# Optimization experiments

Hardware: AMD Instinct MI355X
Metric: run time of the kernel (lower is better)

Reference implementation:

```python
import jax, jax.numpy as jnp
import numpy as np

NUM_GROUPS = 32
EPS = 1e-6


def setup_inputs() -> dict:
    key = jax.random.key(0)
    ks = jax.random.split(key, 4)
    B, C, H, W = 16, 512, 32, 32
    x = jax.random.normal(ks[0], (B, C, H, W), dtype=jnp.float32)
    norm_w = jnp.ones((C,), dtype=jnp.float32)
    norm_b = jnp.zeros((C,), dtype=jnp.float32)
    qkv_w = jax.random.normal(ks[1], (3 * C, C), dtype=jnp.float32) * (1.0 / np.sqrt(C))
    qkv_b = jnp.zeros((3 * C,), dtype=jnp.float32)
    proj_w = jax.random.normal(ks[2], (C, C), dtype=jnp.float32) * (1.0 / np.sqrt(C))
    proj_b = jnp.zeros((C,), dtype=jnp.float32)
    return {"x": x, "norm_w": norm_w, "norm_b": norm_b, "qkv_w": qkv_w,
            "qkv_b": qkv_b, "proj_w": proj_w, "proj_b": proj_b}


def _group_norm(x, w, b):
    B, C, H, W = x.shape
    g = NUM_GROUPS
    xg = x.reshape(B, g, C // g, H * W)
    mu = xg.mean(axis=(2, 3), keepdims=True)
    var = xg.var(axis=(2, 3), keepdims=True)
    xn = (xg - mu) * jax.lax.rsqrt(var + EPS)
    xn = xn.reshape(B, C, H, W)
    return xn * w[None, :, None, None] + b[None, :, None, None]


def reference(x, norm_w, norm_b, qkv_w, qkv_b, proj_w, proj_b):
    B, C, H, W = x.shape
    h = _group_norm(x, norm_w, norm_b)
    # 1x1 conv == channel GEMM
    qkv = jnp.einsum('oc,bchw->bohw', qkv_w, h) + qkv_b[None, :, None, None]
    q, k, v = jnp.split(qkv, 3, axis=1)
    N = H * W
    q = q.reshape(B, C, N)  # (b, c, n)
    k = k.reshape(B, C, N)
    v = v.reshape(B, C, N)
    scale = jnp.asarray(C, x.dtype) ** -0.5
    attn = jnp.einsum('bci,bcj->bij', q, k) * scale  # (b, Nq, Nk)
    attn = jax.nn.softmax(attn, axis=2)
    o = jnp.einsum('bcj,bij->bci', v, attn).reshape(B, C, H, W)
    out = jnp.einsum('oc,bchw->bohw', proj_w, o) + proj_b[None, :, None, None]
    return x + out
```

## Files before the change

### kernel.cpp

```cpp
#include <hip/hip_runtime.h>

typedef unsigned short u16;
typedef __bf16 bf16x8 __attribute__((ext_vector_type(8)));
typedef float f32x4 __attribute__((ext_vector_type(4)));

#define AS1 __attribute__((address_space(1)))
#define AS3 __attribute__((address_space(3)))


__device__ __forceinline__ u16 f2bf(float f) {
  union { float f; unsigned u; } v; v.f = f;
  return (u16)((v.u + 0x7fffu + ((v.u >> 16) & 1u)) >> 16);
}

__device__ __forceinline__ f32x4 mfma16(bf16x8 a, bf16x8 b, f32x4 c) {
  return __builtin_amdgcn_mfma_f32_16x16x32_bf16(a, b, c, 0, 0, 0);
}

__device__ __forceinline__ void stage_tile(const u16* __restrict__ src, size_t ld,
                                           u16* lds, int wv, int lane) {
#pragma unroll
  for (int h2 = 0; h2 < 2; h2++) {
    int rbase = wv * 32 + h2 * 16;
    int row = rbase + (lane >> 2);
    int segd = (lane & 3) ^ ((row >> 1) & 3);
    __builtin_amdgcn_global_load_lds(
        (const AS1 void*)(src + (size_t)row * ld + segd * 8),
        (AS3 void*)(lds + rbase * 32), 16, 0, 0);
  }
}

__device__ __forceinline__ bf16x8 ldsfrag(const u16* lds, int row, int rowq) {
  int q = rowq ^ ((row >> 1) & 3);
  return *(const bf16x8*)(lds + row * 32 + q * 8);
}

template<int NT>
__device__ __forceinline__ void gemm_core3(const u16* __restrict__ A, int lda,
                                           const u16* __restrict__ B, int ldb,
                                           u16* lds, f32x4 (&acc)[4][4],
                                           int wave, int lane) {
  u16* a0 = lds;         u16* a1 = lds + 4096;  u16* a2 = lds + 8192;
  u16* b0 = lds + 12288; u16* b1 = lds + 16384; u16* b2 = lds + 20480;
  int wm = wave >> 1, wn = wave & 1;
  int col = lane & 15, rq = lane >> 4;
#pragma unroll
  for (int m = 0; m < 4; m++)
#pragma unroll
    for (int n = 0; n < 4; n++) acc[m][n] = (f32x4){0.f, 0.f, 0.f, 0.f};

  stage_tile(A, lda, a0, wave, lane);
  stage_tile(B, ldb, b0, wave, lane);
  stage_tile(A + 32, lda, a1, wave, lane);
  stage_tile(B + 32, ldb, b1, wave, lane);

  for (int t = 0; t < NT; t++) {
    if (t < NT - 1) {
      asm volatile("s_waitcnt vmcnt(4)" ::: "memory");
    } else {
      asm volatile("s_waitcnt vmcnt(0)" ::: "memory");
    }
    __builtin_amdgcn_sched_barrier(0);
    __builtin_amdgcn_s_barrier();
    __builtin_amdgcn_sched_barrier(0);
    if (t + 2 < NT) {
      stage_tile(A + (size_t)(t + 2) * 32, lda, a2, wave, lane);
      stage_tile(B + (size_t)(t + 2) * 32, ldb, b2, wave, lane);
    }
    bf16x8 af[4], bfr[4];
#pragma unroll
    for (int n = 0; n < 4; n++) bfr[n] = ldsfrag(b0, wn * 64 + n * 16 + col, rq);
#pragma unroll
    for (int m = 0; m < 4; m++) af[m] = ldsfrag(a0, wm * 64 + m * 16 + col, rq);
#pragma unroll
    for (int m = 0; m < 4; m++)
#pragma unroll
      for (int n = 0; n < 4; n++) acc[m][n] = mfma16(af[m], bfr[n], acc[m][n]);
    u16* ta = a0; a0 = a1; a1 = a2; a2 = ta;
    u16* tb = b0; b0 = b1; b1 = b2; b2 = tb;
  }
}

__device__ __forceinline__ void epi_flush(const u16* lds, u16* gdst, size_t stride, int t) {
#pragma unroll
  for (int pass = 0; pass < 8; pass++) {
    int row = pass * 16 + (t >> 4);
    int ch = (t & 15) * 8;
    uint4 w = *(const uint4*)(lds + row * 132 + ch);
    *(uint4*)(gdst + (size_t)row * stride + ch) = w;
  }
}

__device__ __forceinline__ void stage_half(const u16* __restrict__ src, size_t ld,
                                           u16* ldsbase, int wave, int lane) {
#pragma unroll
  for (int r = 0; r < 2; r++) {
    int rb = (r * 8 + wave) * 8;
    int row = rb + (lane >> 3);
    int seg = (lane & 7) ^ (row & 7);
    __builtin_amdgcn_global_load_lds(
        (const AS1 void*)(src + (size_t)row * ld + seg * 8),
        (AS3 void*)(ldsbase + rb * 64), 16, 0, 0);
  }
}

template<int P>
__device__ __forceinline__ void phase_read(const u16* cA, const u16* cB,
                                           bf16x8 (&af)[2][2], bf16x8 (&bfr)[4][2],
                                           int wm, int wn, int col, int rq) {
  if constexpr (P == 0) {
#pragma unroll
    for (int nf = 0; nf < 4; nf++)
#pragma unroll
      for (int kk = 0; kk < 2; kk++) {
        int row = wn * 64 + nf * 16 + col;
        bfr[nf][kk] = *(const bf16x8*)(cB + row * 64 + (((kk << 2) + rq) ^ (row & 7)) * 8);
      }
  }
#pragma unroll
  for (int i = 0; i < 2; i++)
#pragma unroll
    for (int kk = 0; kk < 2; kk++) {
      int row = wm * 128 + (P * 2 + i) * 16 + col;
      af[i][kk] = *(const bf16x8*)(cA + row * 64 + (((kk << 2) + rq) ^ (row & 7)) * 8);
    }
}

template<int P>
__device__ __forceinline__ void phase_fma(const bf16x8 (&af)[2][2],
                                          const bf16x8 (&bfr)[4][2],
                                          f32x4 (&acc)[8][4]) {
#pragma unroll
  for (int i = 0; i < 2; i++)
#pragma unroll
    for (int kk = 0; kk < 2; kk++)
#pragma unroll
      for (int nf = 0; nf < 4; nf++)
        acc[P * 2 + i][nf] = mfma16(af[i][kk], bfr[nf][kk], acc[P * 2 + i][nf]);
}

#define RUN_PHASE(P, STAGE_CODE, WAIT_CODE)                                  \
  {                                                                          \
    bf16x8 af[2][2];                                                         \
    phase_read<P>(cA, cB, af, bfr, wm, wn, col, rq);                         \
    STAGE_CODE;                                                              \
    WAIT_CODE;                                                               \
    __builtin_amdgcn_sched_barrier(0);                                       \
    __builtin_amdgcn_s_barrier();                                            \
    __builtin_amdgcn_sched_barrier(0);                                       \
    __builtin_amdgcn_s_setprio(1);                                           \
    phase_fma<P>(af, bfr, acc);                                              \
    __builtin_amdgcn_s_setprio(0);                                           \
    __builtin_amdgcn_sched_barrier(0);                                       \
    __builtin_amdgcn_s_barrier();                                            \
    __builtin_amdgcn_sched_barrier(0);                                       \
  }

template<int NT>
__device__ __forceinline__ void gemm8_core(const u16* __restrict__ A, int lda,
                                           const u16* __restrict__ B, int ldb,
                                           u16* lds, f32x4 (&acc)[8][4],
                                           int wave, int lane) {
  u16* Abuf[2] = {lds, lds + 16384};
  u16* Bbuf[2] = {lds + 32768, lds + 49152};
  int wm = wave >> 2, wn = wave & 3;
  int col = lane & 15, rq = lane >> 4;
#pragma unroll
  for (int m = 0; m < 8; m++)
#pragma unroll
    for (int n = 0; n < 4; n++) acc[m][n] = (f32x4){0.f, 0.f, 0.f, 0.f};

  stage_half(A, lda, Abuf[0], wave, lane);
  stage_half(A + 128 * (size_t)lda, lda, Abuf[0] + 8192, wave, lane);
  stage_half(B, ldb, Bbuf[0], wave, lane);
  stage_half(B + 128 * (size_t)ldb, ldb, Bbuf[0] + 8192, wave, lane);
  stage_half(B + 64, ldb, Bbuf[1], wave, lane);
  stage_half(B + 64 + 128 * (size_t)ldb, ldb, Bbuf[1] + 8192, wave, lane);
  asm volatile("s_waitcnt vmcnt(4)" ::: "memory");
  __builtin_amdgcn_sched_barrier(0);
  __builtin_amdgcn_s_barrier();
  __builtin_amdgcn_sched_barrier(0);

  for (int kt = 0; kt < NT; kt++) {
    const u16* cA = Abuf[kt & 1];
    const u16* cB = Bbuf[kt & 1];
    u16* nA = Abuf[(kt + 1) & 1];
    u16* nB = Bbuf[kt & 1];
    const u16* Asrc = A + (size_t)(kt + 1) * 64;
    const u16* Bsrc = B + (size_t)(kt + 2) * 64;
    bool pa = (kt + 1 < NT), pb = (kt + 2 < NT);
    bf16x8 bfr[4][2];
    RUN_PHASE(0, if (pa) stage_half(Asrc, lda, nA, wave, lane), );
    RUN_PHASE(1, if (pa) stage_half(Asrc + 128 * (size_t)lda, lda, nA + 8192, wave, lane), );
    RUN_PHASE(2, if (pb) stage_half(Bsrc, ldb, nB, wave, lane), );
    RUN_PHASE(3, if (pb) stage_half(Bsrc + 128 * (size_t)ldb, ldb, nB + 8192, wave, lane),
              if (pb) { asm volatile("s_waitcnt vmcnt(4)" ::: "memory"); }
              else    { asm volatile("s_waitcnt vmcnt(0)" ::: "memory"); });
  }
}

__global__ __launch_bounds__(256) void gn_fused(const float* __restrict__ x,
                                                const float* __restrict__ gw,
                                                const float* __restrict__ gb,
                                                const float* __restrict__ qkv_w,
                                                const float* __restrict__ proj_w,
                                                u16* __restrict__ h,
                                                u16* __restrict__ wq,
                                                u16* __restrict__ wp) {
  __shared__ float buf[16 * 1032];
  __shared__ float ls[4], lss[4];
  int bg = blockIdx.x;
  int b = bg >> 5, g = bg & 31;
  const float4* p = (const float4*)(x + (size_t)bg * 16384);
  float s = 0.f, ss = 0.f;
  for (int i = threadIdx.x; i < 4096; i += 256) {
    float4 v = p[i];
    int c = i >> 8, n = (i & 255) * 4;
    *(float4*)&buf[c * 1032 + n] = v;
    s  += v.x + v.y + v.z + v.w;
    ss += v.x*v.x + v.y*v.y + v.z*v.z + v.w*v.w;
  }
  {
    int qb = bg * 384;
    for (int u = threadIdx.x; u < 384; u += 256) {
      float4 v = *(const float4*)(qkv_w + (size_t)(qb + u) * 4);
      int o = (qb + u) * 4;
      wq[o] = f2bf(v.x); wq[o+1] = f2bf(v.y); wq[o+2] = f2bf(v.z); wq[o+3] = f2bf(v.w);
    }
    int pb = bg * 128;
    if (threadIdx.x < 128) {
      float4 v = *(const float4*)(proj_w + (size_t)(pb + threadIdx.x) * 4);
      int o = (pb + threadIdx.x) * 4;
      wp[o] = f2bf(v.x); wp[o+1] = f2bf(v.y); wp[o+2] = f2bf(v.z); wp[o+3] = f2bf(v.w);
    }
  }
  for (int d = 32; d; d >>= 1) { s += __shfl_down(s, d); ss += __shfl_down(ss, d); }
  int wv = threadIdx.x >> 6;
  if ((threadIdx.x & 63) == 0) { ls[wv] = s; lss[wv] = ss; }
  __syncthreads();
  float m = (ls[0] + ls[1] + ls[2] + ls[3]) * (1.f / 16384.f);
  float var = (lss[0] + lss[1] + lss[2] + lss[3]) * (1.f / 16384.f) - m * m;
  float r = rsqrtf(var + 1e-6f);
  int c0 = g * 16;
  float w[16], bb[16];
#pragma unroll
  for (int c = 0; c < 16; c++) {
    w[c] = gw[c0 + c] * r;
    bb[c] = gb[c0 + c] - m * w[c];
  }
  for (int n = threadIdx.x; n < 1024; n += 256) {
    u16 o[16];
#pragma unroll
    for (int c = 0; c < 16; c++) o[c] = f2bf(buf[c * 1032 + n] * w[c] + bb[c]);
    u16* dst = h + (((size_t)((b << 10) | n)) << 9) + c0;
    *(uint4*)dst = *(uint4*)o;
    *(uint4*)(dst + 8) = *(uint4*)(o + 8);
  }
}

__global__ __launch_bounds__(256, 3) void gemm_qkv(const u16* __restrict__ A,
                                                   const u16* __restrict__ Bn,
                                                   const float* __restrict__ bias,
                                                   u16* __restrict__ q_nc,
                                                   u16* __restrict__ k_nc,
                                                   u16* __restrict__ v) {
  __shared__ u16 lds[24576];
  int bid = blockIdx.x;
  int xcd = bid & 7, r = bid >> 3;
  int mb = r % 12, nb = xcd * 16 + r / 12;
  int m0 = mb * 128, n0 = nb * 128;
  int t = threadIdx.x, wave = t >> 6, lane = t & 63;
  int wm = wave >> 1, wn = wave & 1;
  int col = lane & 15, rq = lane >> 4;
  f32x4 acc[4][4];
  gemm_core3<16>(A + (size_t)m0 * 512, 512, Bn + (size_t)n0 * 512, 512,
                 lds, acc, wave, lane);
  __syncthreads();
  if (mb < 8) {
#pragma unroll
    for (int i = 0; i < 4; i++)
#pragma unroll
      for (int j = 0; j < 4; j++) {
        int o = m0 + wm * 64 + i * 16 + rq * 4;
        u16 tmp[4];
#pragma unroll
        for (int rr = 0; rr < 4; rr++) tmp[rr] = f2bf(acc[i][j][rr] + bias[o + rr]);
        int bnl = wn * 64 + j * 16 + col;
        int chl = wm * 64 + i * 16 + rq * 4;
        *(uint2*)(lds + bnl * 132 + chl) = *(uint2*)tmp;
      }
    __syncthreads();
    u16* dst = ((mb < 4) ? q_nc : k_nc) + (size_t)n0 * 512 + (m0 & 511);
    epi_flush(lds, dst, 512, t);
  } else {
#pragma unroll
    for (int i = 0; i < 4; i++)
#pragma unroll
      for (int j = 0; j < 4; j++)
#pragma unroll
        for (int rr = 0; rr < 4; rr++) {
          int o = m0 + wm * 64 + i * 16 + rq * 4 + rr;
          int chl = wm * 64 + i * 16 + rq * 4 + rr;
          int bnl = wn * 64 + j * 16 + col;
          lds[chl * 132 + bnl] = f2bf(acc[i][j][rr] + bias[o]);
        }
    __syncthreads();
    u16* dst = v + (size_t)(m0 - 1024) * 16384 + n0;
    epi_flush(lds, dst, 16384, t);
  }
}

__global__ __launch_bounds__(512, 1) void gemm8_s(const u16* __restrict__ q_nc,
                                                  const u16* __restrict__ k_nc,
                                                  u16* __restrict__ E,
                                                  float* __restrict__ part) {
  __shared__ u16 lds[65536];
  int bid = blockIdx.x;
  int xcd = bid & 7, r = bid >> 3;
  int b = xcd * 2 + (r & 1);
  int tile = r >> 1;
  int m0 = (tile >> 2) * 256, n0 = (tile & 3) * 256;
  int t = threadIdx.x, wave = t >> 6, lane = t & 63;
  int wm = wave >> 2, wn = wave & 3;
  int col = lane & 15, rq = lane >> 4;
  f32x4 acc[8][4];
  gemm8_core<8>(q_nc + ((size_t)(b * 1024 + m0)) * 512, 512,
                k_nc + ((size_t)(b * 1024 + n0)) * 512, 512,
                lds, acc, wave, lane);
  float* pb = part + ((size_t)b << 14);
  int idx = (n0 >> 6) + wn;
  const float scale = 0.04419417382415922f;
  __syncthreads();
#pragma unroll
  for (int mf = 0; mf < 8; mf++)
#pragma unroll
    for (int rr = 0; rr < 4; rr++) {
      float e[4], rs = 0.f;
#pragma unroll
      for (int nf = 0; nf < 4; nf++) { e[nf] = __expf(acc[mf][nf][rr] * scale); rs += e[nf]; }
      rs += __shfl_xor(rs, 1); rs += __shfl_xor(rs, 2);
      rs += __shfl_xor(rs, 4); rs += __shfl_xor(rs, 8);
      int il = wm * 128 + mf * 16 + rq * 4 + rr;
      if (col == 0) pb[(m0 + il) * 16 + idx] = rs;
#pragma unroll
      for (int nf = 0; nf < 4; nf++) {
        int j = wn * 64 + nf * 16 + col;
        int jb = (j >> 3) ^ (il & 7);
        lds[il * 256 + (jb << 3) + (j & 7)] = f2bf(e[nf]);
      }
    }
  __syncthreads();
  u16* Eb = E + ((size_t)b << 20) + (size_t)m0 * 1024 + n0;
#pragma unroll
  for (int pass = 0; pass < 16; pass++) {
    int row = pass * 16 + (t >> 5);
    int jbl = t & 31;
    uint4 w = *(const uint4*)(lds + row * 256 + (jbl << 3));
    int jb = jbl ^ (row & 7);
    *(uint4*)(Eb + (size_t)row * 1024 + (jb << 3)) = w;
  }
}

__global__ __launch_bounds__(256, 3) void gemm_pv(const u16* __restrict__ E,
                                                  const u16* __restrict__ v,
                                                  const float* __restrict__ part,
                                                  u16* __restrict__ o_nc) {
  __shared__ u16 lds[24576];
  __shared__ float invs[128];
  int bid = blockIdx.x;
  int xcd = bid & 7, r = bid >> 3;
  int b = xcd * 2 + (r & 1);
  int tile = r >> 1;
  int m0 = (tile >> 2) * 128, n0 = (tile & 3) * 128;
  int t = threadIdx.x, wave = t >> 6, lane = t & 63;
  int wm = wave >> 1, wn = wave & 1;
  int col = lane & 15, rq = lane >> 4;
  f32x4 acc[4][4];
  gemm_core3<32>(E + ((size_t)b << 20) + (size_t)m0 * 1024, 1024,
                 v + (size_t)n0 * 16384 + ((size_t)b << 10), 16384,
                 lds, acc, wave, lane);
  if (t < 128) {
    const float4* p = (const float4*)(part + ((size_t)((b << 10) + m0 + t)) * 16);
    float4 a = p[0], bq = p[1], c = p[2], d = p[3];
    float s = a.x+a.y+a.z+a.w + bq.x+bq.y+bq.z+bq.w + c.x+c.y+c.z+c.w + d.x+d.y+d.z+d.w;
    invs[t] = 1.f / s;
  }
  __syncthreads();
#pragma unroll
  for (int i = 0; i < 4; i++)
#pragma unroll
    for (int rr = 0; rr < 4; rr++) {
      int iil = wm * 64 + i * 16 + rq * 4 + rr;
      float sc = invs[iil];
#pragma unroll
      for (int j = 0; j < 4; j++)
        lds[iil * 132 + wn * 64 + j * 16 + col] = f2bf(acc[i][j][rr] * sc);
    }
  __syncthreads();
  epi_flush(lds, o_nc + ((size_t)(b * 1024 + m0)) * 512 + n0, 512, t);
}

__global__ __launch_bounds__(256, 3) void gemm_proj(const u16* __restrict__ A,
                                                    const u16* __restrict__ Bn,
                                                    const float* __restrict__ bias,
                                                    const float* __restrict__ xres,
                                                    float* __restrict__ outp) {
  __shared__ u16 lds[24576];
  int bid = blockIdx.x;
  int xcd = bid & 7, r = bid >> 3;
  int mb = r & 3, nb = xcd * 16 + (r >> 2);
  int m0 = mb * 128, n0 = nb * 128;
  int t = threadIdx.x, wave = t >> 6, lane = t & 63;
  int wm = wave >> 1, wn = wave & 1;
  int col = lane & 15, rq = lane >> 4;
  f32x4 acc[4][4];
  gemm_core3<16>(A + (size_t)m0 * 512, 512, Bn + (size_t)n0 * 512, 512,
                 lds, acc, wave, lane);
#pragma unroll
  for (int i = 0; i < 4; i++)
#pragma unroll
    for (int j = 0; j < 4; j++)
#pragma unroll
      for (int rr = 0; rr < 4; rr++) {
        int co = m0 + wm * 64 + i * 16 + rq * 4 + rr;
        int bn = n0 + wn * 64 + j * 16 + col;
        int bb = bn >> 10, n = bn & 1023;
        size_t oi = (((size_t)(bb * 512 + co)) << 10) + n;
        outp[oi] = acc[i][j][rr] + bias[co] + xres[oi];
      }
}

extern "C" void kernel_launch(void* const* d_in, const int* in_sizes, int n_in,
                              void* d_out, int out_size, void* d_ws, size_t ws_size,
                              hipStream_t stream) {
  const float* x      = (const float*)d_in[0];
  const float* norm_w = (const float*)d_in[1];
  const float* norm_b = (const float*)d_in[2];
  const float* qkv_w  = (const float*)d_in[3];
  const float* qkv_b  = (const float*)d_in[4];
  const float* proj_w = (const float*)d_in[5];
  const float* proj_b = (const float*)d_in[6];
  float* out = (float*)d_out;

  char* ws = (char*)d_ws;
  size_t off = 0;
  auto alloc = [&](size_t bytes) {
    void* p = ws + off;
    off += (bytes + 255) & ~(size_t)255;
    return p;
  };
  float* part = (float*)alloc((size_t)16384 * 16 * 4);
  u16* wq   = (u16*)alloc((size_t)1536 * 512 * 2);
  u16* wp   = (u16*)alloc((size_t)512 * 512 * 2);
  u16* h    = (u16*)alloc((size_t)16384 * 512 * 2);
  u16* q_nc = (u16*)alloc((size_t)16384 * 512 * 2);
  u16* k_nc = (u16*)alloc((size_t)16384 * 512 * 2);
  u16* v    = (u16*)alloc((size_t)512 * 16384 * 2);
  u16* E    = (u16*)alloc((size_t)16 * 1024 * 1024 * 2);
  u16* o_nc = h;
  (void)in_sizes; (void)n_in; (void)out_size; (void)ws_size;

  gn_fused<<<512, 256, 0, stream>>>(x, norm_w, norm_b, qkv_w, proj_w, h, wq, wp);
  gemm_qkv<<<1536, 256, 0, stream>>>(wq, h, qkv_b, q_nc, k_nc, v);
  gemm8_s<<<256, 512, 0, stream>>>(q_nc, k_nc, E, part);
  gemm_pv<<<512, 256, 0, stream>>>(E, v, part, o_nc);
  gemm_proj<<<512, 256, 0, stream>>>(wp, o_nc, proj_b, x, out);
}
```

Measured before the change: 133.5 us.

## Widen QKV GEMM tiles to 128x256 with double-buffered staging

The QKV projection GEMM now computes 128x256 output tiles per block instead of 128x128, using a new double-buffered gemm_wide core with 32 accumulators per wave. The grid is halved to 768 blocks and the epilogue writes the two 128-column halves through LDS in turn. This raises operand reuse and cuts redundant A-tile loads. In exchange it costs more registers (occupancy bound lowered from 3 to 2), uses two-stage instead of three-stage buffering, and adds extra barriers in the epilogue.

```diff
diff --git a/kernel.cpp b/kernel.cpp
--- a/kernel.cpp
+++ b/kernel.cpp
@@ -22,6 +22,19 @@
 #pragma unroll
   for (int h2 = 0; h2 < 2; h2++) {
     int rbase = wv * 32 + h2 * 16;
+    int row = rbase + (lane >> 2);
+    int segd = (lane & 3) ^ ((row >> 1) & 3);
+    __builtin_amdgcn_global_load_lds(
+        (const AS1 void*)(src + (size_t)row * ld + segd * 8),
+        (AS3 void*)(lds + rbase * 32), 16, 0, 0);
+  }
+}
+
+__device__ __forceinline__ void stage_wide(const u16* __restrict__ src, size_t ld,
+                                           u16* lds, int wv, int lane) {
+#pragma unroll
+  for (int h2 = 0; h2 < 4; h2++) {
+    int rbase = wv * 64 + h2 * 16;
     int row = rbase + (lane >> 2);
     int segd = (lane & 3) ^ ((row >> 1) & 3);
     __builtin_amdgcn_global_load_lds(
@@ -78,6 +91,60 @@
       for (int n = 0; n < 4; n++) acc[m][n] = mfma16(af[m], bfr[n], acc[m][n]);
     u16* ta = a0; a0 = a1; a1 = a2; a2 = ta;
     u16* tb = b0; b0 = b1; b1 = b2; b2 = tb;
+  }
+}
+
+template<int NT>
+__device__ __forceinline__ void gemm_wide(const u16* __restrict__ A, int lda,
+                                          const u16* __restrict__ B, int ldb,
+                                          u16* lds, f32x4 (&acc)[4][8],
+                                          int wave, int lane) {
+  u16* sA0 = lds;          u16* sA1 = lds + 4096;
+  u16* sB0 = lds + 8192;   u16* sB1 = lds + 16384;
+  int wm = wave >> 1, wn = wave & 1;
+  int col = lane & 15, rq = lane >> 4;
+#pragma unroll
+  for (int m = 0; m < 4; m++)
+#pragma unroll
+    for (int n = 0; n < 8; n++) acc[m][n] = (f32x4){0.f, 0.f, 0.f, 0.f};
+
+  stage_tile(A, lda, sA0, wave, lane);
+  stage_wide(B, ldb, sB0, wave, lane);
+  stage_tile(A + 32, lda, sA1, wave, lane);
+  stage_wide(B + 32, ldb, sB1, wave, lane);
+
+  for (int t = 0; t < NT; t++) {
+    u16* cA = (t & 1) ? sA1 : sA0;
+    u16* cB = (t & 1) ? sB1 : sB0;
+    if (t < NT - 1) {
+      asm volatile("s_waitcnt vmcnt(6)" ::: "memory");
+    } else {
+      asm volatile("s_waitcnt vmcnt(0)" ::: "memory");
+    }
+    __builtin_amdgcn_sched_barrier(0);
+    __builtin_amdgcn_s_barrier();
+    __builtin_amdgcn_sched_barrier(0);
+    bf16x8 af[4];
+#pragma unroll
+    for (int m = 0; m < 4; m++) af[m] = ldsfrag(cA, wm * 64 + m * 16 + col, rq);
+#pragma unroll
+    for (int nh = 0; nh < 2; nh++) {
+      bf16x8 bfr[4];
+#pragma unroll
+      for (int n = 0; n < 4; n++)
+        bfr[n] = ldsfrag(cB, wn * 128 + nh * 64 + n * 16 + col, rq);
+#pragma unroll
+      for (int m = 0; m < 4; m++)
+#pragma unroll
+        for (int n = 0; n < 4; n++)
+          acc[m][nh * 4 + n] = mfma16(af[m], bfr[n], acc[m][nh * 4 + n]);
+    }
+    __builtin_amdgcn_sched_barrier(0);
+    __builtin_amdgcn_s_barrier();
+    if (t + 2 < NT) {
+      stage_tile(A + (size_t)(t + 2) * 32, lda, cA, wave, lane);
+      stage_wide(B + (size_t)(t + 2) * 32, ldb, cB, wave, lane);
+    }
   }
 }
 
@@ -258,7 +325,7 @@
   }
 }
 
-__global__ __launch_bounds__(256, 3) void gemm_qkv(const u16* __restrict__ A,
+__global__ __launch_bounds__(256, 2) void gemm_qkv(const u16* __restrict__ A,
                                                    const u16* __restrict__ Bn,
                                                    const float* __restrict__ bias,
                                                    u16* __restrict__ q_nc,
@@ -267,46 +334,57 @@
   __shared__ u16 lds[24576];
   int bid = blockIdx.x;
   int xcd = bid & 7, r = bid >> 3;
-  int mb = r % 12, nb = xcd * 16 + r / 12;
-  int m0 = mb * 128, n0 = nb * 128;
+  int mb = r % 12, nb = xcd * 8 + r / 12;
+  int m0 = mb * 128, n0 = nb * 256;
   int t = threadIdx.x, wave = t >> 6, lane = t & 63;
   int wm = wave >> 1, wn = wave & 1;
   int col = lane & 15, rq = lane >> 4;
-  f32x4 acc[4][4];
-  gemm_core3<16>(A + (size_t)m0 * 512, 512, Bn + (size_t)n0 * 512, 512,
-                 lds, acc, wave, lane);
-  __syncthreads();
+  f32x4 acc[4][8];
+  gemm_wide<16>(A + (size_t)m0 * 512, 512, Bn + (size_t)n0 * 512, 512,
+                lds, acc, wave, lane);
   if (mb < 8) {
-#pragma unroll
-    for (int i = 0; i < 4; i++)
-#pragma unroll
-      for (int j = 0; j < 4; j++) {
-        int o = m0 + wm * 64 + i * 16 + rq * 4;
-        u16 tmp[4];
-#pragma unroll
-        for (int rr = 0; rr < 4; rr++) tmp[rr] = f2bf(acc[i][j][rr] + bias[o + rr]);
-        int bnl = wn * 64 + j * 16 + col;
-        int chl = wm * 64 + i * 16 + rq * 4;
-        *(uint2*)(lds + bnl * 132 + chl) = *(uint2*)tmp;
+    u16* dst = ((mb < 4) ? q_nc : k_nc) + (size_t)n0 * 512 + (m0 & 511);
+#pragma unroll
+    for (int h = 0; h < 2; h++) {
+      __syncthreads();
+      if (wn == h) {
+#pragma unroll
+        for (int m = 0; m < 4; m++)
+#pragma unroll
+          for (int j = 0; j < 8; j++) {
+            int o = m0 + wm * 64 + m * 16 + rq * 4;
+            u16 tmp[4];
+#pragma unroll
+            for (int rr = 0; rr < 4; rr++) tmp[rr] = f2bf(acc[m][j][rr] + bias[o + rr]);
+            int bnl = (j >> 2) * 64 + (j & 3) * 16 + col;
+            int chl = wm * 64 + m * 16 + rq * 4;
+            *(uint2*)(lds + bnl * 132 + chl) = *(uint2*)tmp;
+          }
       }
-    __syncthreads();
-    u16* dst = ((mb < 4) ? q_nc : k_nc) + (size_t)n0 * 512 + (m0 & 511);
-    epi_flush(lds, dst, 512, t);
+      __syncthreads();
+      epi_flush(lds, dst + (size_t)(h * 128) * 512, 512, t);
+    }
   } else {
-#pragma unroll
-    for (int i = 0; i < 4; i++)
-#pragma unroll
-      for (int j = 0; j < 4; j++)
-#pragma unroll
-        for (int rr = 0; rr < 4; rr++) {
-          int o = m0 + wm * 64 + i * 16 + rq * 4 + rr;
-          int chl = wm * 64 + i * 16 + rq * 4 + rr;
-          int bnl = wn * 64 + j * 16 + col;
-          lds[chl * 132 + bnl] = f2bf(acc[i][j][rr] + bias[o]);
-        }
-    __syncthreads();
     u16* dst = v + (size_t)(m0 - 1024) * 16384 + n0;
-    epi_flush(lds, dst, 16384, t);
+#pragma unroll
+    for (int h = 0; h < 2; h++) {
+      __syncthreads();
+      if (wn == h) {
+#pragma unroll
+        for (int m = 0; m < 4; m++)
+#pragma unroll
+          for (int j = 0; j < 8; j++)
+#pragma unroll
+            for (int rr = 0; rr < 4; rr++) {
+              int o = m0 + wm * 64 + m * 16 + rq * 4 + rr;
+              int chl = wm * 64 + m * 16 + rq * 4 + rr;
+              int bnl = (j >> 2) * 64 + (j & 3) * 16 + col;
+              lds[chl * 132 + bnl] = f2bf(acc[m][j][rr] + bias[o]);
+            }
+      }
+      __syncthreads();
+      epi_flush(lds, dst + h * 128, 16384, t);
+    }
   }
 }
 
@@ -461,7 +539,7 @@
   (void)in_sizes; (void)n_in; (void)out_size; (void)ws_size;
 
   gn_fused<<<512, 256, 0, stream>>>(x, norm_w, norm_b, qkv_w, proj_w, h, wq, wp);
-  gemm_qkv<<<1536, 256, 0, stream>>>(wq, h, qkv_b, q_nc, k_nc, v);
+  gemm_qkv<<<768, 256, 0, stream>>>(wq, h, qkv_b, q_nc, k_nc, v);
   gemm8_s<<<256, 512, 0, stream>>>(q_nc, k_nc, E, part);
   gemm_pv<<<512, 256, 0, stream>>>(E, v, part, o_nc);
   gemm_proj<<<512, 256, 0, stream>>>(wp, o_nc, proj_b, x, out);
```

Result: no change. 135.7 us (+1.6%).
